# Performance work log

Hardware: AMD Instinct MI355X
Metric: run time of the kernel (lower is better)

The kernel has to match this reference:

```python
import jax, jax.numpy as jnp
import numpy as np

BEV_H = 128; BEV_W = 128; HEADS = 8; POINTS = 4; NUM_LAYERS = 6
PC = (-51.2, -51.2, -5.0, 51.2, 51.2, 3.0)
EPS = 1e-5


def _layernorm(x, g, b):
    m = x.mean(-1, keepdims=True)
    v = x.var(-1, keepdims=True)
    return (x - m) * jax.lax.rsqrt(v + 1e-5) * g + b


def _bilinear(feat, loc):
    # feat: (H, W, D); loc: (..., 2) normalized xy in [0, 1]; zero padding outside.
    H, W = feat.shape[0], feat.shape[1]
    ix = loc[..., 0] * W - 0.5
    iy = loc[..., 1] * H - 0.5
    x0 = jnp.floor(ix); y0 = jnp.floor(iy)
    fx = ix - x0; fy = iy - y0
    out = 0.0
    for dx in (0, 1):
        for dy in (0, 1):
            xi = x0 + dx; yi = y0 + dy
            w = (fx if dx else 1.0 - fx) * (fy if dy else 1.0 - fy)
            m = (xi >= 0) & (xi < W) & (yi >= 0) & (yi < H)
            xi_c = jnp.clip(xi, 0, W - 1).astype(jnp.int32)
            yi_c = jnp.clip(yi, 0, H - 1).astype(jnp.int32)
            out = out + (w * m)[..., None] * feat[yi_c, xi_c]
    return out


def _deform_grid(q, value, H, W, ref, ow, ob, aw, ab):
    # Deformable attention over a (H, W) grid of values; q: (Nq, C), value: (H*W, C).
    Nq, C = q.shape
    hd = C // HEADS
    v = value.reshape(H, W, HEADS, hd).transpose(2, 0, 1, 3)            # (h, H, W, hd)
    off = (q @ ow + ob).reshape(Nq, HEADS, POINTS, 2)
    loc = ref[:, None, None, :] + off / jnp.array([W, H], q.dtype)      # (Nq, h, P, 2)
    attn = jax.nn.softmax((q @ aw + ab).reshape(Nq, HEADS, POINTS), axis=-1)
    sampled = jax.vmap(_bilinear)(v, loc.transpose(1, 0, 2, 3))         # (h, Nq, P, hd)
    return jnp.einsum('hnpd,nhp->nhd', sampled, attn).reshape(Nq, C)


def _sca(q, feats, ref_cam, valid, ow, ob, aw, ab):
    # Spatial cross-attention: feats (Ncam, h, Hf, Wf, hd), ref_cam (Ncam, Nq, P, 2),
    # valid (Ncam, Nq, P) float mask of in-frustum projections.
    Nq, C = q.shape
    Hf, Wf = feats.shape[2], feats.shape[3]
    off = (q @ ow + ob).reshape(Nq, HEADS, POINTS, 2)
    loc = ref_cam[:, None] + (off / jnp.array([Wf, Hf], q.dtype)).transpose(1, 0, 2, 3)[None]
    # loc: (Ncam, h, Nq, P, 2)
    attn = jax.nn.softmax((q @ aw + ab).reshape(Nq, HEADS, POINTS), axis=-1)
    sampled = jax.vmap(jax.vmap(_bilinear))(feats, loc)                 # (Ncam, h, Nq, P, hd)
    num = jnp.einsum('chnpd,nhp,cnp->nhd', sampled, attn, valid)
    cnt = jnp.maximum(valid.sum((0, 2)), 1.0)                           # (Nq,)
    return (num / cnt[:, None, None]).reshape(Nq, C)


def _forward(image_feats, camera_intrinsics, camera_extrinsics, prev_bev, bev_embed,
             tsa_vw, tsa_vb, tsa_ow, tsa_ob, tsa_aw, tsa_ab, tsa_pw, tsa_pb,
             sca_vw, sca_vb, sca_ow, sca_ob, sca_aw, sca_ab, sca_pw, sca_pb,
             ffn_w1, ffn_b1, ffn_w2, ffn_b2,
             ln1_g, ln1_b, ln2_g, ln2_b, ln3_g, ln3_b):
    Ncam, C, Hf, Wf = image_feats.shape
    hd = C // HEADS
    Nq = BEV_H * BEV_W
    dt = image_feats.dtype
    feats_flat = image_feats.transpose(0, 2, 3, 1).reshape(Ncam * Hf * Wf, C)

    # 2D reference points for temporal self-attention (each query's own cell).
    xs = (jnp.arange(BEV_W, dtype=dt) + 0.5) / BEV_W
    ys = (jnp.arange(BEV_H, dtype=dt) + 0.5) / BEV_H
    gx, gy = jnp.meshgrid(xs, ys)                                       # (H, W) each
    ref2d = jnp.stack([gx.reshape(-1), gy.reshape(-1)], -1)             # (Nq, 2)

    # 3D pillar reference points projected into each camera.
    xm = PC[0] + gx.reshape(-1) * (PC[3] - PC[0])
    ym = PC[1] + gy.reshape(-1) * (PC[4] - PC[1])
    zm = PC[2] + (jnp.arange(POINTS, dtype=dt) + 0.5) / POINTS * (PC[5] - PC[2])
    ref3d = jnp.stack([
        jnp.broadcast_to(xm[:, None], (Nq, POINTS)),
        jnp.broadcast_to(ym[:, None], (Nq, POINTS)),
        jnp.broadcast_to(zm[None, :], (Nq, POINTS)),
        jnp.ones((Nq, POINTS), dt)], -1)                                # (Nq, P, 4)
    ego2cam = jnp.linalg.inv(camera_extrinsics[0])                      # (Ncam, 4, 4)
    pcam = jnp.einsum('cij,npj->cnpi', ego2cam, ref3d)[..., :3]
    img = jnp.einsum('cij,cnpj->cnpi', camera_intrinsics[0], pcam)
    z = img[..., 2]
    un = img[..., 0] / (jnp.maximum(z, EPS) * Wf)
    vn = img[..., 1] / (jnp.maximum(z, EPS) * Hf)
    valid = ((z > EPS) & (un >= 0) & (un <= 1) & (vn >= 0) & (vn <= 1)).astype(dt)
    ref_cam = jnp.stack([un, vn], -1)                                   # (Ncam, Nq, P, 2)

    q = bev_embed                                                       # (Nq, C)
    prev = prev_bev[:, 0, :]                                            # (Nq, C), B = 1
    for l in range(NUM_LAYERS):
        # Temporal self-attention: deformable sampling from prev BEV + current BEV.
        v_prev = prev @ tsa_vw[l] + tsa_vb[l]
        v_cur = q @ tsa_vw[l] + tsa_vb[l]
        a = 0.5 * (_deform_grid(q, v_prev, BEV_H, BEV_W, ref2d, tsa_ow[l], tsa_ob[l], tsa_aw[l], tsa_ab[l])
                   + _deform_grid(q, v_cur, BEV_H, BEV_W, ref2d, tsa_ow[l], tsa_ob[l], tsa_aw[l], tsa_ab[l]))
        q = _layernorm(q + a @ tsa_pw[l] + tsa_pb[l], ln1_g[l], ln1_b[l])
        # Spatial cross-attention over multi-camera image features.
        v_img = (feats_flat @ sca_vw[l] + sca_vb[l]).reshape(Ncam, Hf, Wf, HEADS, hd).transpose(0, 3, 1, 2, 4)
        a = _sca(q, v_img, ref_cam, valid, sca_ow[l], sca_ob[l], sca_aw[l], sca_ab[l])
        q = _layernorm(q + a @ sca_pw[l] + sca_pb[l], ln2_g[l], ln2_b[l])
        # FFN
        a = jax.nn.relu(q @ ffn_w1[l] + ffn_b1[l]) @ ffn_w2[l] + ffn_b2[l]
        q = _layernorm(q + a, ln3_g[l], ln3_b[l])
    return q.T.reshape(1, C, BEV_H, BEV_W)


def setup_inputs() -> dict:
    key = jax.random.key(0)
    ks = iter(jax.random.split(key, 80))
    def nrm(shape, s=0.02):
        return jax.random.normal(next(ks), shape, jnp.float32) * s
    C, L, Ncam, Hf, Wf = 256, NUM_LAYERS, 6, 58, 100
    Nq = BEV_H * BEV_W
    HP, HP2 = HEADS * POINTS, HEADS * POINTS * 2
    # Structured nuScenes-like cameras: 6 yaws at 60 deg, intrinsics at feature-map scale.
    extr = np.zeros((1, Ncam, 4, 4), np.float32)
    for c in range(Ncam):
        t = c * np.pi / 3.0
        f = np.array([np.cos(t), np.sin(t), 0.0])
        xc = np.array([np.sin(t), -np.cos(t), 0.0])
        yc = np.array([0.0, 0.0, -1.0])
        extr[0, c, :3, :3] = np.stack([xc, yc, f], axis=1)
        extr[0, c, :3, 3] = 1.5 * f + np.array([0.0, 0.0, 1.5])
        extr[0, c, 3, 3] = 1.0
    intr = np.zeros((1, Ncam, 3, 3), np.float32)
    intr[0, :, 0, 0] = 80.0; intr[0, :, 1, 1] = 80.0
    intr[0, :, 0, 2] = Wf / 2.0; intr[0, :, 1, 2] = Hf / 2.0
    intr[0, :, 2, 2] = 1.0
    return {
        'image_feats': jax.random.normal(next(ks), (Ncam, C, Hf, Wf), jnp.float32),
        'camera_intrinsics': jnp.asarray(intr),
        'camera_extrinsics': jnp.asarray(extr),
        'prev_bev': jax.random.normal(next(ks), (Nq, 1, C), jnp.float32),
        'bev_embed': nrm((Nq, C)),
        'tsa_vw': nrm((L, C, C)), 'tsa_vb': jnp.zeros((L, C), jnp.float32),
        'tsa_ow': nrm((L, C, HP2)), 'tsa_ob': nrm((L, HP2), 2.0),
        'tsa_aw': nrm((L, C, HP)), 'tsa_ab': jnp.zeros((L, HP), jnp.float32),
        'tsa_pw': nrm((L, C, C)), 'tsa_pb': jnp.zeros((L, C), jnp.float32),
        'sca_vw': nrm((L, C, C)), 'sca_vb': jnp.zeros((L, C), jnp.float32),
        'sca_ow': nrm((L, C, HP2)), 'sca_ob': nrm((L, HP2), 2.0),
        'sca_aw': nrm((L, C, HP)), 'sca_ab': jnp.zeros((L, HP), jnp.float32),
        'sca_pw': nrm((L, C, C)), 'sca_pb': jnp.zeros((L, C), jnp.float32),
        'ffn_w1': nrm((L, C, 2 * C)), 'ffn_b1': jnp.zeros((L, 2 * C), jnp.float32),
        'ffn_w2': nrm((L, 2 * C, C)), 'ffn_b2': jnp.zeros((L, C), jnp.float32),
        'ln1_g': jnp.ones((L, C), jnp.float32), 'ln1_b': jnp.zeros((L, C), jnp.float32),
        'ln2_g': jnp.ones((L, C), jnp.float32), 'ln2_b': jnp.zeros((L, C), jnp.float32),
        'ln3_g': jnp.ones((L, C), jnp.float32), 'ln3_b': jnp.zeros((L, C), jnp.float32),
    }


def reference(image_feats, camera_intrinsics, camera_extrinsics, prev_bev, bev_embed,
              tsa_vw, tsa_vb, tsa_ow, tsa_ob, tsa_aw, tsa_ab, tsa_pw, tsa_pb,
              sca_vw, sca_vb, sca_ow, sca_ob, sca_aw, sca_ab, sca_pw, sca_pb,
              ffn_w1, ffn_b1, ffn_w2, ffn_b2,
              ln1_g, ln1_b, ln2_g, ln2_b, ln3_g, ln3_b):
    return _forward(image_feats, camera_intrinsics, camera_extrinsics, prev_bev, bev_embed,
                    tsa_vw, tsa_vb, tsa_ow, tsa_ob, tsa_aw, tsa_ab, tsa_pw, tsa_pb,
                    sca_vw, sca_vb, sca_ow, sca_ob, sca_aw, sca_ab, sca_pw, sca_pb,
                    ffn_w1, ffn_b1, ffn_w2, ffn_b2,
                    ln1_g, ln1_b, ln2_g, ln2_b, ln3_g, ln3_b)
```

## Files before the change

### kernel.cpp

```cpp
#include <hip/hip_runtime.h>
#include <hip/hip_bf16.h>
#include <math.h>

typedef __hip_bfloat16 bf16;

#define NQ      16384
#define CDIM    256
#define NHEADS  8
#define NPOINTS 4
#define NCAM    6
#define HF      58
#define WF      100
#define HWF     (HF*WF)
#define NFEAT   (NCAM*HWF)
#define HD      32
#define NLAYERS 6

typedef __attribute__((ext_vector_type(8))) short short8;
typedef __attribute__((ext_vector_type(4))) float floatx4;

__device__ __forceinline__ float toF(float x) { return x; }
__device__ __forceinline__ float toF(bf16 x) { return __bfloat162float(x); }
__device__ __forceinline__ void storeD(float* p, float v) { *p = v; }
__device__ __forceinline__ void storeD(bf16* p, float v) { *p = __float2bfloat16(v); }

__device__ __forceinline__ float bfLo(unsigned u) { return __uint_as_float(u << 16); }
__device__ __forceinline__ float bfHi(unsigned u) { return __uint_as_float(u & 0xffff0000u); }

__device__ __forceinline__ void gload_lds16(const bf16* g, bf16* l) {
    __builtin_amdgcn_global_load_lds(
        (const __attribute__((address_space(1))) void*)(g),
        (__attribute__((address_space(3))) void*)(l), 16, 0, 0);
}


template <typename DT, bool RELU, bool STAGE, bool ZF>
__global__ __launch_bounds__(256) void gemm_mfma(
    const bf16* __restrict__ A, const bf16* __restrict__ BT,
    const float* __restrict__ bias, DT* __restrict__ D,
    int M, int N, int K, size_t sB, size_t sBias, size_t sD)
{
    int z, bn, bm;
    if (ZF) {
        int nwg = gridDim.x;
        int logical = (blockIdx.x & 7) * (nwg >> 3) + (blockIdx.x >> 3);
        int idx = logical % (2 * NLAYERS);
        bm = (logical / (2 * NLAYERS)) * 128;
        z  = idx % NLAYERS;
        bn = (idx / NLAYERS) * 128;
    } else {
        z  = blockIdx.z;
        bn = blockIdx.x * 128;
        bm = blockIdx.y * 128;
    }
    BT += (size_t)z * sB;
    bias += (size_t)z * sBias;
    D += (size_t)z * sD;

    __shared__ bf16 smem[STAGE ? 128 * 136 : 128 * 64];
    bf16* As = smem;
    bf16* Bs = smem + 128 * 32;

    int tid = threadIdx.x;
    int lane = tid & 63, w = tid >> 6;
    int wm = w & 1, wn = w >> 1;
    int l15 = lane & 15, quad = lane >> 4;

    floatx4 acc[4][4];
#pragma unroll
    for (int i = 0; i < 4; i++)
#pragma unroll
        for (int j = 0; j < 4; j++)
            acc[i][j] = (floatx4){0.f, 0.f, 0.f, 0.f};

    int rsub = lane >> 2;
    int kc   = (((lane & 3) ^ ((rsub >> 1) & 3))) * 8;
    int sw   = (l15 >> 1) & 3;

    for (int k0 = 0; k0 < K; k0 += 32) {
#pragma unroll
        for (int h = 0; h < 2; h++) {
            int r0 = w * 32 + h * 16;
            int gm = bm + r0 + rsub;
            if (gm > M - 1) gm = M - 1;
            gload_lds16(A + (size_t)gm * K + k0 + kc, &As[r0 * 32]);
            gload_lds16(BT + (size_t)(bn + r0 + rsub) * K + k0 + kc, &Bs[r0 * 32]);
        }
        __syncthreads();

        short8 a[4], b[4];
#pragma unroll
        for (int i = 0; i < 4; i++)
            a[i] = *(const short8*)(&As[(wm * 64 + i * 16 + l15) * 32 + (quad ^ sw) * 8]);
#pragma unroll
        for (int j = 0; j < 4; j++)
            b[j] = *(const short8*)(&Bs[(wn * 64 + j * 16 + l15) * 32 + (quad ^ sw) * 8]);
#pragma unroll
        for (int i = 0; i < 4; i++)
#pragma unroll
            for (int j = 0; j < 4; j++)
                acc[i][j] = __builtin_amdgcn_mfma_f32_16x16x32_bf16(
                    a[i], b[j], acc[i][j], 0, 0, 0);
        __syncthreads();
    }

    if (STAGE) {
#pragma unroll
        for (int i = 0; i < 4; i++) {
#pragma unroll
            for (int j = 0; j < 4; j++) {
                int col = wn * 64 + j * 16 + l15;
                float bv = bias[bn + col];
#pragma unroll
                for (int r = 0; r < 4; r++) {
                    int row = wm * 64 + i * 16 + quad * 4 + r;
                    float v = acc[i][j][r] + bv;
                    if (RELU) v = fmaxf(v, 0.f);
                    smem[row * 136 + col] = __float2bfloat16(v);
                }
            }
        }
        __syncthreads();
        int lr0 = tid >> 4;
        int ck  = tid & 15;
#pragma unroll
        for (int pass = 0; pass < 8; pass++) {
            int lr = pass * 16 + lr0;
            int gm = bm + lr;
            if (gm < M) {
                uint4 v = *(const uint4*)(&smem[lr * 136 + ck * 8]);
                *(uint4*)((bf16*)D + (size_t)gm * N + bn + ck * 8) = v;
            }
        }
    } else {
#pragma unroll
        for (int i = 0; i < 4; i++) {
#pragma unroll
            for (int j = 0; j < 4; j++) {
                int col = bn + wn * 64 + j * 16 + l15;
                float bv = bias[col];
#pragma unroll
                for (int r = 0; r < 4; r++) {
                    int row = bm + wm * 64 + i * 16 + quad * 4 + r;
                    if (row < M) {
                        float v = acc[i][j][r] + bv;
                        if (RELU) v = fmaxf(v, 0.f);
                        storeD(&D[(size_t)row * N + col], v);
                    }
                }
            }
        }
    }
}

__global__ __launch_bounds__(256) void gemm_off(
    const bf16* __restrict__ A, const bf16* __restrict__ BT,
    const float* __restrict__ bias, float* __restrict__ D)
{
    __shared__ bf16 As[64 * 32];
    __shared__ bf16 Bs[64 * 32];

    int tid = threadIdx.x;
    int lane = tid & 63, w = tid >> 6;
    int l15 = lane & 15, quad = lane >> 4;
    int bm = blockIdx.y * 64, bn = blockIdx.x * 64;

    floatx4 acc[4];
#pragma unroll
    for (int j = 0; j < 4; j++)
        acc[j] = (floatx4){0.f, 0.f, 0.f, 0.f};

    int rsub = lane >> 2;
    int kc   = (((lane & 3) ^ ((rsub >> 1) & 3))) * 8;
    int sw   = (l15 >> 1) & 3;

    for (int k0 = 0; k0 < 256; k0 += 32) {
        gload_lds16(A + (size_t)(bm + w * 16 + rsub) * 256 + k0 + kc, &As[w * 16 * 32]);
        gload_lds16(BT + (size_t)(bn + w * 16 + rsub) * 256 + k0 + kc, &Bs[w * 16 * 32]);
        __syncthreads();

        short8 a = *(const short8*)(&As[(w * 16 + l15) * 32 + (quad ^ sw) * 8]);
        short8 b[4];
#pragma unroll
        for (int j = 0; j < 4; j++)
            b[j] = *(const short8*)(&Bs[(j * 16 + l15) * 32 + (quad ^ sw) * 8]);
#pragma unroll
        for (int j = 0; j < 4; j++)
            acc[j] = __builtin_amdgcn_mfma_f32_16x16x32_bf16(a, b[j], acc[j], 0, 0, 0);
        __syncthreads();
    }

#pragma unroll
    for (int j = 0; j < 4; j++) {
        int col = bn + j * 16 + l15;
        float bv = bias[col];
#pragma unroll
        for (int r = 0; r < 4; r++) {
            int row = bm + w * 16 + quad * 4 + r;
            D[(size_t)row * 128 + col] = acc[j][r] + bv;
        }
    }
}

__global__ __launch_bounds__(256) void gemm_tsa(
    const bf16* __restrict__ A, const bf16* __restrict__ BT,
    const float* __restrict__ bias,
    bf16* __restrict__ vgrid, float* __restrict__ offlog)
{
    int bn3 = blockIdx.x;
    int bm = blockIdx.y * 128;
    if (bn3 == 2 && bm < NQ) return;
    int bn = bn3 * 128;

    __shared__ bf16 As[128 * 32];
    __shared__ bf16 Bs[128 * 32];

    int tid = threadIdx.x;
    int lane = tid & 63, w = tid >> 6;
    int wm = w & 1, wn = w >> 1;
    int l15 = lane & 15, quad = lane >> 4;

    floatx4 acc[4][4];
#pragma unroll
    for (int i = 0; i < 4; i++)
#pragma unroll
        for (int j = 0; j < 4; j++)
            acc[i][j] = (floatx4){0.f, 0.f, 0.f, 0.f};

    int rsub = lane >> 2;
    int kc   = (((lane & 3) ^ ((rsub >> 1) & 3))) * 8;
    int sw   = (l15 >> 1) & 3;

    for (int k0 = 0; k0 < 256; k0 += 32) {
#pragma unroll
        for (int h = 0; h < 2; h++) {
            int r0 = w * 32 + h * 16;
            gload_lds16(A + (size_t)(bm + r0 + rsub) * 256 + k0 + kc, &As[r0 * 32]);
            gload_lds16(BT + (size_t)(bn + r0 + rsub) * 256 + k0 + kc, &Bs[r0 * 32]);
        }
        __syncthreads();

        short8 a[4], b[4];
#pragma unroll
        for (int i = 0; i < 4; i++)
            a[i] = *(const short8*)(&As[(wm * 64 + i * 16 + l15) * 32 + (quad ^ sw) * 8]);
#pragma unroll
        for (int j = 0; j < 4; j++)
            b[j] = *(const short8*)(&Bs[(wn * 64 + j * 16 + l15) * 32 + (quad ^ sw) * 8]);
#pragma unroll
        for (int i = 0; i < 4; i++)
#pragma unroll
            for (int j = 0; j < 4; j++)
                acc[i][j] = __builtin_amdgcn_mfma_f32_16x16x32_bf16(
                    a[i], b[j], acc[i][j], 0, 0, 0);
        __syncthreads();
    }

#pragma unroll
    for (int i = 0; i < 4; i++) {
#pragma unroll
        for (int j = 0; j < 4; j++) {
            int col = bn + wn * 64 + j * 16 + l15;
            float bv = bias[col];
#pragma unroll
            for (int r = 0; r < 4; r++) {
                int row = bm + wm * 64 + i * 16 + quad * 4 + r;
                float v = acc[i][j][r] + bv;
                if (bn3 < 2) {
                    int n = row & (NQ - 1);
                    int cur = row >= NQ;
                    size_t idx = ((size_t)n * 64 + (col >> 2)) * 8 + cur * 4 + (col & 3);
                    vgrid[idx] = __float2bfloat16(v);
                } else {
                    offlog[(size_t)(row - NQ) * 128 + (col - 256)] = v;
                }
            }
        }
    }
}

__global__ __launch_bounds__(512) void gemm_ln(
    const bf16* __restrict__ A, const bf16* __restrict__ BT,
    const float* __restrict__ bias,
    bf16* __restrict__ qb,
    const float* __restrict__ g, const float* __restrict__ b,
    int K)
{
    __shared__ bf16 As[64 * 32];
    __shared__ bf16 Bs[256 * 32];
    __shared__ float red[2][64][4];
    __shared__ float stats[2][64];

    int tid = threadIdx.x;
    int lane = tid & 63, w = tid >> 6;
    int wm = w & 1, wn = w >> 1;
    int l15 = lane & 15, quad = lane >> 4;
    int bm = blockIdx.x * 64;

    floatx4 acc[2][4];
#pragma unroll
    for (int i = 0; i < 2; i++)
#pragma unroll
        for (int j = 0; j < 4; j++)
            acc[i][j] = (floatx4){0.f, 0.f, 0.f, 0.f};

    int rsub = lane >> 2;
    int kc   = (((lane & 3) ^ ((rsub >> 1) & 3))) * 8;
    int sw   = (l15 >> 1) & 3;

    for (int k0 = 0; k0 < K; k0 += 32) {
#pragma unroll
        for (int h = 0; h < 2; h++) {
            int r0 = w * 32 + h * 16;
            gload_lds16(BT + (size_t)(r0 + rsub) * K + k0 + kc, &Bs[r0 * 32]);
        }
        if (w < 4)
            gload_lds16(A + (size_t)(bm + w * 16 + rsub) * K + k0 + kc,
                        &As[w * 16 * 32]);
        __syncthreads();

        short8 a[2], bfr[4];
#pragma unroll
        for (int i = 0; i < 2; i++)
            a[i] = *(const short8*)(&As[(wm * 32 + i * 16 + l15) * 32 + (quad ^ sw) * 8]);
#pragma unroll
        for (int j = 0; j < 4; j++)
            bfr[j] = *(const short8*)(&Bs[(wn * 64 + j * 16 + l15) * 32 + (quad ^ sw) * 8]);
#pragma unroll
        for (int i = 0; i < 2; i++)
#pragma unroll
            for (int j = 0; j < 4; j++)
                acc[i][j] = __builtin_amdgcn_mfma_f32_16x16x32_bf16(
                    a[i], bfr[j], acc[i][j], 0, 0, 0);
        __syncthreads();
    }

    float x[2][4][4];
#pragma unroll
    for (int i = 0; i < 2; i++) {
#pragma unroll
        for (int j = 0; j < 4; j++) {
            int col = wn * 64 + j * 16 + l15;
            float bv = bias[col];
#pragma unroll
            for (int r = 0; r < 4; r++) {
                int row = bm + wm * 32 + i * 16 + quad * 4 + r;
                x[i][j][r] = toF(qb[(size_t)row * CDIM + col]) + acc[i][j][r] + bv;
            }
        }
    }
#pragma unroll
    for (int i = 0; i < 2; i++) {
#pragma unroll
        for (int r = 0; r < 4; r++) {
            float s = x[i][0][r] + x[i][1][r] + x[i][2][r] + x[i][3][r];
            float sq = x[i][0][r] * x[i][0][r] + x[i][1][r] * x[i][1][r] +
                       x[i][2][r] * x[i][2][r] + x[i][3][r] * x[i][3][r];
#pragma unroll
            for (int m = 1; m < 16; m <<= 1) {
                s += __shfl_xor(s, m);
                sq += __shfl_xor(sq, m);
            }
            if (l15 == 0) {
                int rl = wm * 32 + i * 16 + quad * 4 + r;
                red[0][rl][wn] = s;
                red[1][rl][wn] = sq;
            }
        }
    }
    __syncthreads();
    if (tid < 64) {
        float s = red[0][tid][0] + red[0][tid][1] + red[0][tid][2] + red[0][tid][3];
        float sq = red[1][tid][0] + red[1][tid][1] + red[1][tid][2] + red[1][tid][3];
        float mean = s * (1.f / CDIM);
        float var = fmaxf(sq * (1.f / CDIM) - mean * mean, 0.f);
        stats[0][tid] = mean;
        stats[1][tid] = rsqrtf(var + 1e-5f);
    }
    __syncthreads();
#pragma unroll
    for (int i = 0; i < 2; i++) {
#pragma unroll
        for (int j = 0; j < 4; j++) {
            int col = wn * 64 + j * 16 + l15;
            float gc = g[col], bc = b[col];
#pragma unroll
            for (int r = 0; r < 4; r++) {
                int rl = wm * 32 + i * 16 + quad * 4 + r;
                int row = bm + rl;
                float y = (x[i][j][r] - stats[0][rl]) * stats[1][rl] * gc + bc;
                qb[(size_t)row * CDIM + col] = __float2bfloat16(y);
            }
        }
    }
}

__global__ void wt_cvt_kernel(const float* __restrict__ W, bf16* __restrict__ WT,
                              int K, int N)
{
    __shared__ float tile[32][33];
    int l = blockIdx.z;
    const float* Wl = W + (size_t)l * K * N;
    bf16* WTl = WT + (size_t)l * K * N;
    int k0 = blockIdx.x * 32, n0 = blockIdx.y * 32;
    int tx = threadIdx.x, ty = threadIdx.y;
    for (int i = 0; i < 32; i += 8)
        tile[ty + i][tx] = Wl[(size_t)(k0 + ty + i) * N + n0 + tx];
    __syncthreads();
    for (int i = 0; i < 32; i += 8)
        WTl[(size_t)(n0 + ty + i) * K + k0 + tx] = __float2bfloat16(tile[tx][ty + i]);
}

__global__ void pack_tsa_kernel(const float* __restrict__ vw, const float* __restrict__ vb,
                                const float* __restrict__ ow, const float* __restrict__ ob,
                                const float* __restrict__ aw, const float* __restrict__ ab,
                                bf16* __restrict__ WT, float* __restrict__ BIAS)
{
    int n = blockIdx.x;
    int l = blockIdx.y;
    int k = threadIdx.x;
    float v = 0.f;
    if (n < 256)      v = vw[((size_t)l * 256 + k) * 256 + n];
    else if (n < 320) v = ow[((size_t)l * 256 + k) * 64 + (n - 256)];
    else if (n < 352) v = aw[((size_t)l * 256 + k) * 32 + (n - 320)];
    WT[((size_t)l * 384 + n) * 256 + k] = __float2bfloat16(v);
    if (k == 0) {
        float bv = 0.f;
        if (n < 256)      bv = vb[l * 256 + n];
        else if (n < 320) bv = ob[l * 64 + (n - 256)];
        else if (n < 352) bv = ab[l * 32 + (n - 320)];
        BIAS[l * 384 + n] = bv;
    }
}

__global__ void pack_offattn_kernel(const float* __restrict__ ow, const float* __restrict__ ob,
                                    const float* __restrict__ aw, const float* __restrict__ ab,
                                    bf16* __restrict__ WT, float* __restrict__ BIAS)
{
    int l = blockIdx.y;
    int n = blockIdx.x;
    int k = threadIdx.x;
    float v = 0.f;
    if (n < 64)      v = ow[((size_t)l * 256 + k) * 64 + n];
    else if (n < 96) v = aw[((size_t)l * 256 + k) * 32 + (n - 64)];
    WT[((size_t)l * 128 + n) * 256 + k] = __float2bfloat16(v);
    if (k == 0) {
        float bv = 0.f;
        if (n < 64)      bv = ob[l * 64 + n];
        else if (n < 96) bv = ab[l * 32 + (n - 64)];
        BIAS[l * 128 + n] = bv;
    }
}

__global__ void feats_cvt_kernel(const float* __restrict__ in, bf16* __restrict__ outT)
{
    __shared__ float tile[32][33];
    int c = blockIdx.z;
    int r0 = blockIdx.x * 32, ch0 = blockIdx.y * 32;
    int tx = threadIdx.x, ty = threadIdx.y;
    for (int i = 0; i < 32; i += 8) {
        int r = r0 + tx, ch = ch0 + ty + i;
        tile[ty + i][tx] = (r < HWF) ? in[((size_t)c * CDIM + ch) * HWF + r] : 0.f;
    }
    __syncthreads();
    for (int i = 0; i < 32; i += 8) {
        int r = r0 + ty + i, ch = ch0 + tx;
        if (r < HWF)
            outT[((size_t)c * HWF + r) * CDIM + ch] = __float2bfloat16(tile[tx][ty + i]);
    }
}

__global__ __launch_bounds__(256) void cvt_bf16_kernel(const float* __restrict__ in,
                                                       bf16* __restrict__ out, int n)
{
    int i = blockIdx.x * 256 + threadIdx.x;
    if (i < n) out[i] = __float2bfloat16(in[i]);
}

__global__ void invert4_kernel(const float* __restrict__ extr, float* __restrict__ ego)
{
    int c = threadIdx.x;
    if (c >= NCAM) return;
    float a[4][8];
    for (int i = 0; i < 4; i++)
        for (int j = 0; j < 4; j++) {
            a[i][j] = extr[c * 16 + i * 4 + j];
            a[i][4 + j] = (i == j) ? 1.f : 0.f;
        }
    for (int col = 0; col < 4; col++) {
        int piv = col;
        float best = fabsf(a[col][col]);
        for (int r = col + 1; r < 4; r++) {
            float v = fabsf(a[r][col]);
            if (v > best) { best = v; piv = r; }
        }
        if (piv != col)
            for (int j = 0; j < 8; j++) {
                float t = a[col][j]; a[col][j] = a[piv][j]; a[piv][j] = t;
            }
        float inv = 1.f / a[col][col];
        for (int j = 0; j < 8; j++) a[col][j] *= inv;
        for (int r = 0; r < 4; r++) {
            if (r == col) continue;
            float f = a[r][col];
            for (int j = 0; j < 8; j++) a[r][j] -= f * a[col][j];
        }
    }
    for (int i = 0; i < 4; i++)
        for (int j = 0; j < 4; j++)
            ego[c * 16 + i * 4 + j] = a[i][4 + j];
}

__global__ __launch_bounds__(256) void refcam_compact_kernel(
    const float* __restrict__ ego, const float* __restrict__ intr,
    float4* __restrict__ entries, int* __restrict__ cnt)
{
    int n = blockIdx.x * 256 + threadIdx.x;
    if (n >= NQ) return;

    float gx = ((n & 127) + 0.5f) / 128.0f;
    float gy = ((n >> 7) + 0.5f) / 128.0f;
    float xm = -51.2f + gx * 102.4f;
    float ym = -51.2f + gy * 102.4f;

    float4* out = entries + (size_t)n * 24;
    int k = 0;
    for (int c = 0; c < NCAM; c++) {
        const float* E = ego + c * 16;
        const float* I = intr + c * 9;
#pragma unroll
        for (int p = 0; p < NPOINTS; p++) {
            float zm = -5.0f + (p + 0.5f) * 2.0f;
            float pc[3];
#pragma unroll
            for (int i = 0; i < 3; i++)
                pc[i] = E[i * 4 + 0] * xm + E[i * 4 + 1] * ym + E[i * 4 + 2] * zm + E[i * 4 + 3];
            float im[3];
#pragma unroll
            for (int i = 0; i < 3; i++)
                im[i] = I[i * 3 + 0] * pc[0] + I[i * 3 + 1] * pc[1] + I[i * 3 + 2] * pc[2];
            float z = im[2];
            float zc = fmaxf(z, 1e-5f);
            float un = im[0] / (zc * (float)WF);
            float vn = im[1] / (zc * (float)HF);
            if (z > 1e-5f && un >= 0.f && un <= 1.f && vn >= 0.f && vn <= 1.f) {
                out[k] = make_float4(un, vn, __int_as_float(c * 4 + p), 0.f);
                k++;
            }
        }
    }
    cnt[n] = k;
}

__global__ __launch_bounds__(256) void tsa_sample_kernel(
    const bf16* __restrict__ vgrid, const float* __restrict__ offlog,
    bf16* __restrict__ outA)
{
    int blk = blockIdx.x;
    int qq = (blk & 7) * 512 + (blk >> 3);
    int t = threadIdx.x;
    int n = qq * 4 + (t >> 6);
    int r = t & 63;
    int h = r >> 3;
    int dq = r & 7;
    int col = h * HD + dq * 4;
    int q8 = h * 8 + dq;

    const float* fl = offlog + (size_t)n * 128;
    const float* lg = fl + 64 + h * 4;
    float l0 = lg[0], l1 = lg[1], l2 = lg[2], l3 = lg[3];
    float mx = fmaxf(fmaxf(l0, l1), fmaxf(l2, l3));
    float e0 = expf(l0 - mx), e1 = expf(l1 - mx), e2 = expf(l2 - mx), e3 = expf(l3 - mx);
    float inv = 1.f / (e0 + e1 + e2 + e3);
    float w[4] = { e0 * inv, e1 * inv, e2 * inv, e3 * inv };

    const float* of = fl + h * 8;
    float rx = ((n & 127) + 0.5f) / 128.f;
    float ry = ((n >> 7) + 0.5f) / 128.f;

    float a0 = 0.f, a1 = 0.f, a2 = 0.f, a3 = 0.f;
#pragma unroll
    for (int p = 0; p < NPOINTS; p++) {
        float lx = rx + of[p * 2] * (1.f / 128.f);
        float ly = ry + of[p * 2 + 1] * (1.f / 128.f);
        float ix = lx * 128.f - 0.5f;
        float iy = ly * 128.f - 0.5f;
        float xf = floorf(ix), yf = floorf(iy);
        float fx = ix - xf, fy = iy - yf;
        int x0 = (int)xf, y0 = (int)yf;
#pragma unroll
        for (int dy = 0; dy < 2; dy++) {
            int yi = y0 + dy;
            if (yi < 0 || yi >= 128) continue;
            float wy = dy ? fy : 1.f - fy;
#pragma unroll
            for (int dx = 0; dx < 2; dx++) {
                int xi = x0 + dx;
                if (xi < 0 || xi >= 128) continue;
                float wgt = w[p] * wy * (dx ? fx : 1.f - fx);
                size_t idx = ((size_t)(yi * 128 + xi) * 64 + q8) * 8;
                uint4 v = *(const uint4*)(vgrid + idx);
                a0 += wgt * (bfLo(v.x) + bfLo(v.z));
                a1 += wgt * (bfHi(v.x) + bfHi(v.z));
                a2 += wgt * (bfLo(v.y) + bfLo(v.w));
                a3 += wgt * (bfHi(v.y) + bfHi(v.w));
            }
        }
    }
    union { bf16 b[4]; uint2 u; } pk;
    pk.b[0] = __float2bfloat16(0.5f * a0);
    pk.b[1] = __float2bfloat16(0.5f * a1);
    pk.b[2] = __float2bfloat16(0.5f * a2);
    pk.b[3] = __float2bfloat16(0.5f * a3);
    *(uint2*)(outA + (size_t)n * CDIM + col) = pk.u;
}

__global__ __launch_bounds__(256) void sca_sample_kernel(
    const bf16* __restrict__ vimg, const float* __restrict__ offlog,
    const float4* __restrict__ entries, const int* __restrict__ cnt,
    bf16* __restrict__ outA)
{
    int blk = blockIdx.x;
    int qo = (blk & 7) * 256 + (blk >> 3);
    int t = threadIdx.x;
    int n = qo * 8 + (t >> 5);
    int r = t & 31;
    int h = r >> 2;
    int d8 = r & 3;
    int col = h * HD + d8 * 8;

    const float* fl = offlog + (size_t)n * 128;
    const float* lg = fl + 64 + h * 4;
    float l0 = lg[0], l1 = lg[1], l2 = lg[2], l3 = lg[3];
    float mx = fmaxf(fmaxf(l0, l1), fmaxf(l2, l3));
    float e0 = expf(l0 - mx), e1 = expf(l1 - mx), e2 = expf(l2 - mx), e3 = expf(l3 - mx);
    float inv = 1.f / (e0 + e1 + e2 + e3);
    float w[4] = { e0 * inv, e1 * inv, e2 * inv, e3 * inv };

    const float* of = fl + h * 8;
    float ox[4], oy[4];
#pragma unroll
    for (int p = 0; p < NPOINTS; p++) {
        ox[p] = of[p * 2] * (1.f / (float)WF);
        oy[p] = of[p * 2 + 1] * (1.f / (float)HF);
    }

    int ne = cnt[n];
    const float4* ent = entries + (size_t)n * 24;

    float a0 = 0.f, a1 = 0.f, a2 = 0.f, a3 = 0.f;
    float a4 = 0.f, a5 = 0.f, a6 = 0.f, a7 = 0.f;
    for (int e = 0; e < ne; e++) {
        float4 E = ent[e];
        int cp = __float_as_int(E.z);
        int c = cp >> 2, p = cp & 3;
        float lx = E.x + ox[p];
        float ly = E.y + oy[p];
        float ix = lx * (float)WF - 0.5f;
        float iy = ly * (float)HF - 0.5f;
        float xf = floorf(ix), yf = floorf(iy);
        float fx = ix - xf, fy = iy - yf;
        int x0 = (int)xf, y0 = (int)yf;
        float wp_ = w[p];
        const bf16* vb = vimg + (size_t)c * HWF * CDIM;
#pragma unroll
        for (int dy = 0; dy < 2; dy++) {
            int yi = y0 + dy;
            if (yi < 0 || yi >= HF) continue;
            float wy = dy ? fy : 1.f - fy;
#pragma unroll
            for (int dx = 0; dx < 2; dx++) {
                int xi = x0 + dx;
                if (xi < 0 || xi >= WF) continue;
                float wgt = wp_ * wy * (dx ? fx : 1.f - fx);
                uint4 u = *(const uint4*)(vb + (size_t)(yi * WF + xi) * CDIM + col);
                a0 += wgt * bfLo(u.x);
                a1 += wgt * bfHi(u.x);
                a2 += wgt * bfLo(u.y);
                a3 += wgt * bfHi(u.y);
                a4 += wgt * bfLo(u.z);
                a5 += wgt * bfHi(u.z);
                a6 += wgt * bfLo(u.w);
                a7 += wgt * bfHi(u.w);
            }
        }
    }
    float ic = 1.f / fmaxf((float)ne, 1.f);
    union { bf16 b[8]; uint4 u; } pk;
    pk.b[0] = __float2bfloat16(a0 * ic);
    pk.b[1] = __float2bfloat16(a1 * ic);
    pk.b[2] = __float2bfloat16(a2 * ic);
    pk.b[3] = __float2bfloat16(a3 * ic);
    pk.b[4] = __float2bfloat16(a4 * ic);
    pk.b[5] = __float2bfloat16(a5 * ic);
    pk.b[6] = __float2bfloat16(a6 * ic);
    pk.b[7] = __float2bfloat16(a7 * ic);
    *(uint4*)(outA + (size_t)n * CDIM + col) = pk.u;
}

__global__ void out_transpose_kernel(const bf16* __restrict__ qb, float* __restrict__ out)
{
    __shared__ float tile[32][33];
    int n0 = blockIdx.x * 32;
    int c0 = blockIdx.y * 32;
    int tx = threadIdx.x, ty = threadIdx.y;
    for (int i = 0; i < 32; i += 8)
        tile[ty + i][tx] = toF(qb[(size_t)(n0 + ty + i) * CDIM + c0 + tx]);
    __syncthreads();
    for (int i = 0; i < 32; i += 8)
        out[(size_t)(c0 + ty + i) * NQ + n0 + tx] = tile[tx][ty + i];
}

extern "C" void kernel_launch(void* const* d_in, const int* in_sizes, int n_in,
                              void* d_out, int out_size, void* d_ws, size_t ws_size,
                              hipStream_t stream)
{
    const float* image_feats = (const float*)d_in[0];
    const float* intr        = (const float*)d_in[1];
    const float* extr        = (const float*)d_in[2];
    const float* prev_bev    = (const float*)d_in[3];
    const float* bev_embed   = (const float*)d_in[4];
    const float* tsa_vw = (const float*)d_in[5];
    const float* tsa_vb = (const float*)d_in[6];
    const float* tsa_ow = (const float*)d_in[7];
    const float* tsa_ob = (const float*)d_in[8];
    const float* tsa_aw = (const float*)d_in[9];
    const float* tsa_ab = (const float*)d_in[10];
    const float* tsa_pw = (const float*)d_in[11];
    const float* tsa_pb = (const float*)d_in[12];
    const float* sca_vw = (const float*)d_in[13];
    const float* sca_vb = (const float*)d_in[14];
    const float* sca_ow = (const float*)d_in[15];
    const float* sca_ob = (const float*)d_in[16];
    const float* sca_aw = (const float*)d_in[17];
    const float* sca_ab = (const float*)d_in[18];
    const float* sca_pw = (const float*)d_in[19];
    const float* sca_pb = (const float*)d_in[20];
    const float* ffn_w1 = (const float*)d_in[21];
    const float* ffn_b1 = (const float*)d_in[22];
    const float* ffn_w2 = (const float*)d_in[23];
    const float* ffn_b2 = (const float*)d_in[24];
    const float* ln1_g  = (const float*)d_in[25];
    const float* ln1_b  = (const float*)d_in[26];
    const float* ln2_g  = (const float*)d_in[27];
    const float* ln2_b  = (const float*)d_in[28];
    const float* ln3_g  = (const float*)d_in[29];
    const float* ln3_b  = (const float*)d_in[30];

    char* wp = (char*)d_ws;
    auto alloc = [&](size_t bytes) -> void* {
        void* r = (void*)wp;
        wp += (bytes + 255) & ~(size_t)255;
        return r;
    };
    bf16*  prevbf = (bf16*) alloc((size_t)NQ * CDIM * 2);
    bf16*  qb     = (bf16*) alloc((size_t)NQ * CDIM * 2);
    bf16*  attnA  = (bf16*) alloc((size_t)NQ * CDIM * 2);
    float* offlog = (float*)alloc((size_t)NQ * 128 * 4);
    float4* entries = (float4*)alloc((size_t)NQ * 24 * 16);
    int*   entcnt = (int*)  alloc((size_t)NQ * 4);
    float* ego    = (float*)alloc(128 * 4);
    bf16*  featsT = (bf16*) alloc((size_t)NFEAT * CDIM * 2);
    bf16*  pwT  = (bf16*)alloc((size_t)NLAYERS * 65536 * 2);
    bf16*  svwT = (bf16*)alloc((size_t)NLAYERS * 65536 * 2);
    bf16*  spwT = (bf16*)alloc((size_t)NLAYERS * 65536 * 2);
    bf16*  w1T  = (bf16*)alloc((size_t)NLAYERS * 131072 * 2);
    bf16*  w2T  = (bf16*)alloc((size_t)NLAYERS * 131072 * 2);
    bf16*  ptwT = (bf16*)alloc((size_t)NLAYERS * 384 * 256 * 2);
    float* ptb  = (float*)alloc((size_t)NLAYERS * 384 * 4);
    bf16*  sowT = (bf16*)alloc((size_t)NLAYERS * 32768 * 2);
    float* sobF = (float*)alloc((size_t)NLAYERS * 128 * 4);
    bf16*  vgrid = (bf16*)alloc((size_t)NQ * CDIM * 2 * 2);
    bf16*  vimg6 = (bf16*)alloc((size_t)NLAYERS * NFEAT * CDIM * 2);

    bf16* hidden = featsT;

    dim3 blk32(32, 8);

    cvt_bf16_kernel<<<(NQ * CDIM + 255) / 256, 256, 0, stream>>>(bev_embed, qb, NQ * CDIM);
    cvt_bf16_kernel<<<(NQ * CDIM + 255) / 256, 256, 0, stream>>>(prev_bev, prevbf, NQ * CDIM);
    invert4_kernel<<<1, 64, 0, stream>>>(extr, ego);
    refcam_compact_kernel<<<NQ / 256, 256, 0, stream>>>(ego, intr, entries, entcnt);
    {
        dim3 g((HWF + 31) / 32, CDIM / 32, NCAM);
        feats_cvt_kernel<<<g, blk32, 0, stream>>>(image_feats, featsT);
    }
    wt_cvt_kernel<<<dim3(8, 8,  NLAYERS), blk32, 0, stream>>>(tsa_pw, pwT,  256, 256);
    wt_cvt_kernel<<<dim3(8, 8,  NLAYERS), blk32, 0, stream>>>(sca_vw, svwT, 256, 256);
    wt_cvt_kernel<<<dim3(8, 8,  NLAYERS), blk32, 0, stream>>>(sca_pw, spwT, 256, 256);
    wt_cvt_kernel<<<dim3(8, 16, NLAYERS), blk32, 0, stream>>>(ffn_w1, w1T, 256, 512);
    wt_cvt_kernel<<<dim3(16, 8, NLAYERS), blk32, 0, stream>>>(ffn_w2, w2T, 512, 256);
    pack_tsa_kernel<<<dim3(384, NLAYERS), 256, 0, stream>>>(
        tsa_vw, tsa_vb, tsa_ow, tsa_ob, tsa_aw, tsa_ab, ptwT, ptb);
    pack_offattn_kernel<<<dim3(128, NLAYERS), 256, 0, stream>>>(
        sca_ow, sca_ob, sca_aw, sca_ab, sowT, sobF);
    gemm_mfma<bf16, false, true, true><<<dim3(2 * NLAYERS * 272), 256, 0, stream>>>(
        featsT, svwT, sca_vb, vimg6, NFEAT, CDIM, CDIM,
        65536, 256, (size_t)NFEAT * CDIM);

    for (int l = 0; l < NLAYERS; l++) {
        gemm_tsa<<<dim3(3, 2 * NQ / 128), 256, 0, stream>>>(
            prevbf, ptwT + (size_t)l * 98304, ptb + l * 384, vgrid, offlog);
        tsa_sample_kernel<<<NQ / 4, 256, 0, stream>>>(vgrid, offlog, attnA);
        gemm_ln<<<NQ / 64, 512, 0, stream>>>(
            attnA, pwT + (size_t)l * 65536, tsa_pb + l * CDIM,
            qb, ln1_g + l * CDIM, ln1_b + l * CDIM, CDIM);

        gemm_off<<<dim3(2, NQ / 64), 256, 0, stream>>>(
            qb, sowT + (size_t)l * 32768, sobF + l * 128, offlog);
        sca_sample_kernel<<<NQ / 8, 256, 0, stream>>>(
            vimg6 + (size_t)l * NFEAT * CDIM, offlog, entries, entcnt, attnA);
        gemm_ln<<<NQ / 64, 512, 0, stream>>>(
            attnA, spwT + (size_t)l * 65536, sca_pb + l * CDIM,
            qb, ln2_g + l * CDIM, ln2_b + l * CDIM, CDIM);

        gemm_mfma<bf16, true, true, false><<<dim3(4, NQ / 128, 1), 256, 0, stream>>>(
            qb, w1T + (size_t)l * 131072, ffn_b1 + l * 512, hidden, NQ, 512, CDIM, 0, 0, 0);
        gemm_ln<<<NQ / 64, 512, 0, stream>>>(
            hidden, w2T + (size_t)l * 131072, ffn_b2 + l * CDIM,
            qb, ln3_g + l * CDIM, ln3_b + l * CDIM, 512);
    }

    {
        dim3 g(NQ / 32, CDIM / 32);
        out_transpose_kernel<<<g, blk32, 0, stream>>>(qb, (float*)d_out);
    }
}
```

Before: 978.1 us.

## Fold TSA value averaging into a precomputed mean of prev and current BEV

Temporal self-attention sampled values from both prev_bev and the current query, then averaged the two. Because the value projection is linear, the change projects the mean of prev_bev and the query once, which halves the value GEMM rows and the vgrid size and drops the extra gather and 0.5 scaling. The mean is produced by a small init kernel and afterwards fused into the FFN LayerNorm epilogue. It also writes vgrid in a plain row-major layout through LDS-staged coalesced 16-byte stores. The cost is an extra bf16 rounding of the mean and an extra prev_bev read and qmean write per layer.

```diff
diff --git a/kernel.cpp b/kernel.cpp
--- a/kernel.cpp
+++ b/kernel.cpp
@@ -203,17 +203,18 @@
 }
 
 __global__ __launch_bounds__(256) void gemm_tsa(
-    const bf16* __restrict__ A, const bf16* __restrict__ BT,
-    const float* __restrict__ bias,
+    const bf16* __restrict__ qmean, const bf16* __restrict__ qb,
+    const bf16* __restrict__ BT, const float* __restrict__ bias,
     bf16* __restrict__ vgrid, float* __restrict__ offlog)
 {
     int bn3 = blockIdx.x;
     int bm = blockIdx.y * 128;
-    if (bn3 == 2 && bm < NQ) return;
     int bn = bn3 * 128;
-
-    __shared__ bf16 As[128 * 32];
-    __shared__ bf16 Bs[128 * 32];
+    const bf16* A = (bn3 == 2) ? qb : qmean;
+
+    __shared__ bf16 smem[128 * 136];
+    bf16* As = smem;
+    bf16* Bs = smem + 128 * 32;
 
     int tid = threadIdx.x;
     int lane = tid & 63, w = tid >> 6;
@@ -256,35 +257,53 @@
         __syncthreads();
     }
 
-#pragma unroll
-    for (int i = 0; i < 4; i++) {
-#pragma unroll
-        for (int j = 0; j < 4; j++) {
-            int col = bn + wn * 64 + j * 16 + l15;
-            float bv = bias[col];
-#pragma unroll
-            for (int r = 0; r < 4; r++) {
-                int row = bm + wm * 64 + i * 16 + quad * 4 + r;
-                float v = acc[i][j][r] + bv;
-                if (bn3 < 2) {
-                    int n = row & (NQ - 1);
-                    int cur = row >= NQ;
-                    size_t idx = ((size_t)n * 64 + (col >> 2)) * 8 + cur * 4 + (col & 3);
-                    vgrid[idx] = __float2bfloat16(v);
-                } else {
-                    offlog[(size_t)(row - NQ) * 128 + (col - 256)] = v;
+    if (bn3 < 2) {
+#pragma unroll
+        for (int i = 0; i < 4; i++) {
+#pragma unroll
+            for (int j = 0; j < 4; j++) {
+                int col = wn * 64 + j * 16 + l15;
+                float bv = bias[bn + col];
+#pragma unroll
+                for (int r = 0; r < 4; r++) {
+                    int row = wm * 64 + i * 16 + quad * 4 + r;
+                    smem[row * 136 + col] = __float2bfloat16(acc[i][j][r] + bv);
                 }
             }
         }
-    }
-}
-
+        __syncthreads();
+        int lr0 = tid >> 4;
+        int ck  = tid & 15;
+#pragma unroll
+        for (int pass = 0; pass < 8; pass++) {
+            int lr = pass * 16 + lr0;
+            uint4 v = *(const uint4*)(&smem[lr * 136 + ck * 8]);
+            *(uint4*)(vgrid + (size_t)(bm + lr) * 256 + bn + ck * 8) = v;
+        }
+    } else {
+#pragma unroll
+        for (int i = 0; i < 4; i++) {
+#pragma unroll
+            for (int j = 0; j < 4; j++) {
+                int col = wn * 64 + j * 16 + l15;
+                float bv = bias[256 + col];
+#pragma unroll
+                for (int r = 0; r < 4; r++) {
+                    int row = bm + wm * 64 + i * 16 + quad * 4 + r;
+                    offlog[(size_t)row * 128 + col] = acc[i][j][r] + bv;
+                }
+            }
+        }
+    }
+}
+
+template <bool QM>
 __global__ __launch_bounds__(512) void gemm_ln(
     const bf16* __restrict__ A, const bf16* __restrict__ BT,
     const float* __restrict__ bias,
     bf16* __restrict__ qb,
     const float* __restrict__ g, const float* __restrict__ b,
-    int K)
+    int K, const bf16* __restrict__ prevb, bf16* __restrict__ qmean)
 {
     __shared__ bf16 As[64 * 32];
     __shared__ bf16 Bs[256 * 32];
@@ -390,9 +409,30 @@
                 int row = bm + rl;
                 float y = (x[i][j][r] - stats[0][rl]) * stats[1][rl] * gc + bc;
                 qb[(size_t)row * CDIM + col] = __float2bfloat16(y);
-            }
-        }
-    }
+                if (QM)
+                    qmean[(size_t)row * CDIM + col] = __float2bfloat16(
+                        0.5f * (toF(prevb[(size_t)row * CDIM + col]) + y));
+            }
+        }
+    }
+}
+
+__global__ __launch_bounds__(256) void qmean_kernel(
+    const bf16* __restrict__ a, const bf16* __restrict__ b, bf16* __restrict__ o)
+{
+    int i = blockIdx.x * 256 + threadIdx.x;
+    short8 va = ((const short8*)a)[i];
+    short8 vb = ((const short8*)b)[i];
+    short8 vo;
+#pragma unroll
+    for (int j = 0; j < 8; j++) {
+        float fa = __uint_as_float(((unsigned)(unsigned short)va[j]) << 16);
+        float fb = __uint_as_float(((unsigned)(unsigned short)vb[j]) << 16);
+        union { bf16 h; short s; } u;
+        u.h = __float2bfloat16(0.5f * (fa + fb));
+        vo[j] = u.s;
+    }
+    ((short8*)o)[i] = vo;
 }
 
 __global__ void wt_cvt_kernel(const float* __restrict__ W, bf16* __restrict__ WT,
@@ -564,7 +604,6 @@
     int h = r >> 3;
     int dq = r & 7;
     int col = h * HD + dq * 4;
-    int q8 = h * 8 + dq;
 
     const float* fl = offlog + (size_t)n * 128;
     const float* lg = fl + 64 + h * 4;
@@ -598,20 +637,19 @@
                 int xi = x0 + dx;
                 if (xi < 0 || xi >= 128) continue;
                 float wgt = w[p] * wy * (dx ? fx : 1.f - fx);
-                size_t idx = ((size_t)(yi * 128 + xi) * 64 + q8) * 8;
-                uint4 v = *(const uint4*)(vgrid + idx);
-                a0 += wgt * (bfLo(v.x) + bfLo(v.z));
-                a1 += wgt * (bfHi(v.x) + bfHi(v.z));
-                a2 += wgt * (bfLo(v.y) + bfLo(v.w));
-                a3 += wgt * (bfHi(v.y) + bfHi(v.w));
+                uint2 v = *(const uint2*)(vgrid + (size_t)(yi * 128 + xi) * 256 + col);
+                a0 += wgt * bfLo(v.x);
+                a1 += wgt * bfHi(v.x);
+                a2 += wgt * bfLo(v.y);
+                a3 += wgt * bfHi(v.y);
             }
         }
     }
     union { bf16 b[4]; uint2 u; } pk;
-    pk.b[0] = __float2bfloat16(0.5f * a0);
-    pk.b[1] = __float2bfloat16(0.5f * a1);
-    pk.b[2] = __float2bfloat16(0.5f * a2);
-    pk.b[3] = __float2bfloat16(0.5f * a3);
+    pk.b[0] = __float2bfloat16(a0);
+    pk.b[1] = __float2bfloat16(a1);
+    pk.b[2] = __float2bfloat16(a2);
+    pk.b[3] = __float2bfloat16(a3);
     *(uint2*)(outA + (size_t)n * CDIM + col) = pk.u;
 }
 
@@ -755,6 +793,7 @@
     };
     bf16*  prevbf = (bf16*) alloc((size_t)NQ * CDIM * 2);
     bf16*  qb     = (bf16*) alloc((size_t)NQ * CDIM * 2);
+    bf16*  qmeanb = (bf16*) alloc((size_t)NQ * CDIM * 2);
     bf16*  attnA  = (bf16*) alloc((size_t)NQ * CDIM * 2);
     float* offlog = (float*)alloc((size_t)NQ * 128 * 4);
     float4* entries = (float4*)alloc((size_t)NQ * 24 * 16);
@@ -770,7 +809,7 @@
     float* ptb  = (float*)alloc((size_t)NLAYERS * 384 * 4);
     bf16*  sowT = (bf16*)alloc((size_t)NLAYERS * 32768 * 2);
     float* sobF = (float*)alloc((size_t)NLAYERS * 128 * 4);
-    bf16*  vgrid = (bf16*)alloc((size_t)NQ * CDIM * 2 * 2);
+    bf16*  vgrid = (bf16*)alloc((size_t)NQ * CDIM * 2);
     bf16*  vimg6 = (bf16*)alloc((size_t)NLAYERS * NFEAT * CDIM * 2);
 
     bf16* hidden = featsT;
@@ -779,6 +818,7 @@
 
     cvt_bf16_kernel<<<(NQ * CDIM + 255) / 256, 256, 0, stream>>>(bev_embed, qb, NQ * CDIM);
     cvt_bf16_kernel<<<(NQ * CDIM + 255) / 256, 256, 0, stream>>>(prev_bev, prevbf, NQ * CDIM);
+    qmean_kernel<<<NQ * CDIM / 8 / 256, 256, 0, stream>>>(prevbf, qb, qmeanb);
     invert4_kernel<<<1, 64, 0, stream>>>(extr, ego);
     refcam_compact_kernel<<<NQ / 256, 256, 0, stream>>>(ego, intr, entries, entcnt);
     {
@@ -799,26 +839,31 @@
         65536, 256, (size_t)NFEAT * CDIM);
 
     for (int l = 0; l < NLAYERS; l++) {
-        gemm_tsa<<<dim3(3, 2 * NQ / 128), 256, 0, stream>>>(
-            prevbf, ptwT + (size_t)l * 98304, ptb + l * 384, vgrid, offlog);
+        gemm_tsa<<<dim3(3, NQ / 128), 256, 0, stream>>>(
+            qmeanb, qb, ptwT + (size_t)l * 98304, ptb + l * 384, vgrid, offlog);
         tsa_sample_kernel<<<NQ / 4, 256, 0, stream>>>(vgrid, offlog, attnA);
-        gemm_ln<<<NQ / 64, 512, 0, stream>>>(
+        gemm_ln<false><<<NQ / 64, 512, 0, stream>>>(
             attnA, pwT + (size_t)l * 65536, tsa_pb + l * CDIM,
-            qb, ln1_g + l * CDIM, ln1_b + l * CDIM, CDIM);
+            qb, ln1_g + l * CDIM, ln1_b + l * CDIM, CDIM, nullptr, nullptr);
 
         gemm_off<<<dim3(2, NQ / 64), 256, 0, stream>>>(
             qb, sowT + (size_t)l * 32768, sobF + l * 128, offlog);
         sca_sample_kernel<<<NQ / 8, 256, 0, stream>>>(
             vimg6 + (size_t)l * NFEAT * CDIM, offlog, entries, entcnt, attnA);
-        gemm_ln<<<NQ / 64, 512, 0, stream>>>(
+        gemm_ln<false><<<NQ / 64, 512, 0, stream>>>(
             attnA, spwT + (size_t)l * 65536, sca_pb + l * CDIM,
-            qb, ln2_g + l * CDIM, ln2_b + l * CDIM, CDIM);
+            qb, ln2_g + l * CDIM, ln2_b + l * CDIM, CDIM, nullptr, nullptr);
 
         gemm_mfma<bf16, true, true, false><<<dim3(4, NQ / 128, 1), 256, 0, stream>>>(
             qb, w1T + (size_t)l * 131072, ffn_b1 + l * 512, hidden, NQ, 512, CDIM, 0, 0, 0);
-        gemm_ln<<<NQ / 64, 512, 0, stream>>>(
-            hidden, w2T + (size_t)l * 131072, ffn_b2 + l * CDIM,
-            qb, ln3_g + l * CDIM, ln3_b + l * CDIM, 512);
+        if (l < NLAYERS - 1)
+            gemm_ln<true><<<NQ / 64, 512, 0, stream>>>(
+                hidden, w2T + (size_t)l * 131072, ffn_b2 + l * CDIM,
+                qb, ln3_g + l * CDIM, ln3_b + l * CDIM, 512, prevbf, qmeanb);
+        else
+            gemm_ln<false><<<NQ / 64, 512, 0, stream>>>(
+                hidden, w2T + (size_t)l * 131072, ffn_b2 + l * CDIM,
+                qb, ln3_g + l * CDIM, ln3_b + l * CDIM, 512, nullptr, nullptr);
     }
 
     {
```

Result: faster. 933.6 us (-4.5%).
